# Kernel tuning notes

Hardware: AMD Instinct MI355X
Metric: run time of the kernel (lower is better)

Reference implementation:

```python
import math
import jax, jax.numpy as jnp
import numpy as np

N_ATOMS = 500000
N_TYPES = 16
N_FEAT = 64
N_CENTER = 40000
N_NEIGH = 6
H1, H2 = 128, 64
CUTOFF = 3.5
D_IN = 3 + 3 * N_FEAT  # 195

# static off-diagonal (j,k) pairs, row-major == torch's ~eye boolean mask order
_JJ, _KK = np.nonzero(~np.eye(N_NEIGH, dtype=bool))


def setup_inputs() -> dict:
    key = jax.random.key(0)
    ks = jax.random.split(key, 9)
    atoms_xyz = jax.random.normal(ks[0], (N_ATOMS, 3), dtype=jnp.float32) * 5.0
    atom_type_idx = jax.random.randint(ks[1], (N_ATOMS,), 0, N_TYPES)
    embed_table = jax.random.normal(ks[2], (N_TYPES, N_FEAT), dtype=jnp.float32)
    atom_i_idx = jax.random.randint(ks[3], (N_CENTER,), 0, N_ATOMS)
    # distinct neighbor indices per row (real neighbor lists never repeat an atom)
    base = jax.random.randint(ks[4], (N_CENTER, 1), 0, N_ATOMS)
    atom_j_idx = (base + jnp.arange(N_NEIGH)) % N_ATOMS
    # center->neighbor distances, strictly positive (within angular cutoff scale)
    dist_ij = 0.5 + 3.0 * jax.random.uniform(ks[5], (N_CENTER, N_NEIGH), dtype=jnp.float32)
    W1 = jax.random.normal(ks[6], (H1, D_IN), dtype=jnp.float32) / np.sqrt(D_IN).astype(np.float32)
    b1 = jnp.zeros((H1,), dtype=jnp.float32)
    W2 = jax.random.normal(ks[7], (H2, H1), dtype=jnp.float32) / np.sqrt(H1).astype(np.float32)
    b2 = jnp.zeros((H2,), dtype=jnp.float32)
    return dict(atoms_xyz=atoms_xyz, embed_table=embed_table, dist_ij=dist_ij,
                W1=W1, b1=b1, W2=W2, b2=b2,
                atom_type_idx=atom_type_idx, atom_i_idx=atom_i_idx, atom_j_idx=atom_j_idx)


def _ang_input(atoms_xyz, embed_table, dist_ij, atom_type_idx, atom_i_idx, atom_j_idx):
    # Build angular descriptor directly on off-diagonal (j,k) triples -> [C, T, 3+3F]
    xyz_j = atoms_xyz[atom_j_idx]                       # [C, N, 3]
    diff = xyz_j[:, _JJ] - xyz_j[:, _KK]                # [C, T, 3]
    d_jk = jnp.sqrt(jnp.sum(diff * diff, axis=-1))      # [C, T]
    dij = dist_ij[:, _JJ]                                # [C, T]
    dik = dist_ij[:, _KK]
    mx = jnp.maximum(dij, dik)
    mn = jnp.minimum(dij, dik)
    d_jk_norm = (d_jk - mx + mn) / (2.0 * mn)
    e_i = embed_table[atom_type_idx[atom_i_idx]]        # [C, F]
    e_n = embed_table[atom_type_idx[atom_j_idx]]        # [C, N, F]
    e_j = e_n[:, _JJ]                                    # [C, T, F]
    e_k = e_n[:, _KK]
    ang = jnp.concatenate([
        dij[..., None], dik[..., None], d_jk_norm[..., None],
        jnp.broadcast_to(e_i[:, None, :], e_j.shape),
        e_j / dij[..., None],
        e_k / dik[..., None],
    ], axis=-1)                                          # [C, T, 3+3F]
    return ang


def reference(atoms_xyz, embed_table, dist_ij, W1, b1, W2, b2,
              atom_type_idx, atom_i_idx, atom_j_idx):
    ang = _ang_input(atoms_xyz, embed_table, dist_ij,
                     atom_type_idx, atom_i_idx, atom_j_idx)   # [C, T, D_IN]
    C, T, _ = ang.shape
    x = ang.reshape(-1, D_IN)
    x = jax.nn.celu(x @ W1.T + b1)
    x = jax.nn.celu(x @ W2.T + b2)
    out = x.reshape(C, T, H2)
    # smooth angular cutoff from the ij, ik distance columns
    fc = 0.5 * jnp.cos(math.pi * jnp.clip(ang[:, :, 0:2] / CUTOFF, 0.0, 1.0)) + 0.5
    fc = jnp.prod(fc, axis=-1, keepdims=True)            # [C, T, 1]
    desc = jnp.sum(out * fc, axis=1)                     # [C, H2]
    return desc
```

## Files before the change

kernel.cpp:

```cpp
#include <hip/hip_runtime.h>
#include <hip/hip_bf16.h>

typedef __attribute__((ext_vector_type(8))) short bfrag;
typedef __attribute__((ext_vector_type(4))) float facc;
typedef __attribute__((ext_vector_type(4))) int ivec4;
typedef __attribute__((ext_vector_type(4))) short svec4;

#define DIN 195
#define H1 128
#define H2 64
#define CPB 4
#define ROWS 128
#define TPB 512
#define X1STR 136
#define TLSTR 40
#define VSTR 72

#define W1T_ELEMS (8*7*64*8)
#define W2T_ELEMS (4*4*64*8)

__device__ __forceinline__ short f2bf(float v) {
    __hip_bfloat16 h = __float2bfloat16(v);
    return __builtin_bit_cast(short, h);
}

__global__ void prep_weights(const float* __restrict__ W1, const float* __restrict__ W2,
                             __hip_bfloat16* __restrict__ W1t, __hip_bfloat16* __restrict__ W2t) {
    int i = blockIdx.x * 256 + threadIdx.x;
    if (i < W1T_ELEMS) {
        int e = i & 7, l = (i >> 3) & 63;
        int k0 = (i >> 9) % 7, mt = (i >> 9) / 7;
        int h = mt * 16 + (l & 15);
        int kp = k0 * 32 + ((l >> 4) & 3) * 8 + e;
        float v = 0.f;
        if (kp < 192)      v = W1[h * DIN + 3 + kp];
        else if (kp < 195) v = W1[h * DIN + (kp - 192)];
        W1t[i] = __float2bfloat16(v);
    } else {
        int j = i - W1T_ELEMS;
        if (j < W2T_ELEMS) {
            int e = j & 7, l = (j >> 3) & 63;
            int k0 = (j >> 9) & 3, mm = j >> 11;
            int h = mm * 16 + (l & 15);
            int k = k0 * 32 + ((l >> 4) & 3) * 8 + e;
            W2t[j] = __float2bfloat16(W2[h * H1 + k]);
        }
    }
}

template<bool PREP>
__global__ __launch_bounds__(TPB, 4) void angnet(
    const float* __restrict__ atoms_xyz,
    const float* __restrict__ embed,
    const float* __restrict__ dist_ij,
    const float* __restrict__ b1,
    const float* __restrict__ b2,
    const int* __restrict__ atype,
    const int* __restrict__ aidx,
    const int* __restrict__ ajdx,
    const __hip_bfloat16* __restrict__ W1t,
    const __hip_bfloat16* __restrict__ W2t,
    const float* __restrict__ W1f,
    const float* __restrict__ W2f,
    float* __restrict__ out)
{
    __shared__ __align__(16) __hip_bfloat16 x1s[ROWS][X1STR];
    __shared__ __align__(16) __hip_bfloat16 tail[ROWS][TLSTR];
    __shared__ __align__(16) __hip_bfloat16 vst[CPB][7][VSTR];
    __shared__ float fcs[ROWS];
    __shared__ float dstage[CPB][6];
    __shared__ float xyzs[CPB][6][3];
    __shared__ int   tidx[CPB][7];

    const int tid = threadIdx.x;
    const int C0 = blockIdx.x * CPB;

    {
        ivec4 zz = {0, 0, 0, 0};
        for (int i = tid; i < ROWS * TLSTR / 8; i += TPB)
            ((ivec4*)tail)[i] = zz;
    }
    if (tid < CPB * 7) {
        int c = tid / 7, r = tid % 7;
        tidx[c][r] = (r == 6) ? atype[aidx[C0 + c]] : atype[ajdx[(C0 + c) * 6 + r]];
    } else if (tid < CPB * 7 + CPB * 18) {
        int q = tid - CPB * 7; int c = q / 18, rr = q % 18; int n = rr / 3, ax = rr % 3;
        xyzs[c][n][ax] = atoms_xyz[(long)ajdx[(C0 + c) * 6 + n] * 3 + ax];
    } else if (tid < CPB * 7 + CPB * 18 + CPB * 6) {
        int q = tid - CPB * 7 - CPB * 18; int c = q / 6, n = q % 6;
        dstage[c][n] = dist_ij[(C0 + c) * 6 + n];
    }
    __syncthreads();

    if (tid < CPB * 7 * 8) {
        int c = tid / 56, rem = tid % 56, v = rem / 8, ch = rem % 8;
        int ti = tidx[c][v];
        float sc = (v < 6) ? (1.0f / dstage[c][v]) : 1.0f;
        const float* ep = &embed[ti * 64 + ch * 8];
        float4 e0 = *(const float4*)ep;
        float4 e1 = *(const float4*)(ep + 4);
        bfrag t;
        t[0] = f2bf(e0.x * sc); t[1] = f2bf(e0.y * sc);
        t[2] = f2bf(e0.z * sc); t[3] = f2bf(e0.w * sc);
        t[4] = f2bf(e1.x * sc); t[5] = f2bf(e1.y * sc);
        t[6] = f2bf(e1.z * sc); t[7] = f2bf(e1.w * sc);
        *(bfrag*)&vst[c][v][ch * 8] = t;
    } else if (tid >= 256 && tid < 256 + CPB * 30) {
        int q = tid - 256; int c = q / 30, t = q % 30;
        int j = t / 5, k2 = t - j * 5, k = k2 + (k2 >= j ? 1 : 0);
        float dij = dstage[c][j], dik = dstage[c][k];
        float dx = xyzs[c][j][0] - xyzs[c][k][0];
        float dy = xyzs[c][j][1] - xyzs[c][k][1];
        float dz = xyzs[c][j][2] - xyzs[c][k][2];
        float djk = sqrtf(dx * dx + dy * dy + dz * dz);
        float mx = fmaxf(dij, dik), mn = fminf(dij, dik);
        float djkn = (djk - mx + mn) / (2.0f * mn);
        int r = c * 32 + t;
        tail[r][0] = __float2bfloat16(dij);
        tail[r][1] = __float2bfloat16(dik);
        tail[r][2] = __float2bfloat16(djkn);
        const float PIF = 3.14159265358979323846f;
        float ca = __cosf(PIF * (dij * (1.0f / 3.5f)));
        float cb = __cosf(PIF * (dik * (1.0f / 3.5f)));
        fcs[r] = (0.5f * ca + 0.5f) * (0.5f * cb + 0.5f);
    } else if (tid >= 376 && tid < 384) {
        int p = tid - 376;
        fcs[(p >> 1) * 32 + 30 + (p & 1)] = 0.f;
    }
    __syncthreads();

    const int w = tid >> 6, l = tid & 63, lr = l & 15, lq = l >> 4;

    int jn[8], kn[8];
    #pragma unroll
    for (int n = 0; n < 8; ++n) {
        int t = (n & 1) * 16 + lr;
        int j = t / 5, k2 = t - j * 5, k = k2 + (k2 >= j ? 1 : 0);
        if (t >= 30) { j = 0; k = 0; }
        jn[n] = j; kn[n] = k;
    }
    facc a1[8];
    #pragma unroll
    for (int n = 0; n < 8; ++n) a1[n] = (facc){0.f, 0.f, 0.f, 0.f};

    #pragma unroll
    for (int k0 = 0; k0 < 7; ++k0) {
        bfrag Af;
        if (PREP) {
            Af = *(const bfrag*)&W1t[(w * 7 + k0) * 512 + l * 8];
        } else {
            #pragma unroll
            for (int e = 0; e < 8; ++e) {
                int kp = k0 * 32 + lq * 8 + e;
                int h = w * 16 + lr;
                float v = 0.f;
                if (kp < 192)      v = W1f[h * DIN + 3 + kp];
                else if (kp < 195) v = W1f[h * DIN + kp - 192];
                Af[e] = f2bf(v);
            }
        }
        #pragma unroll
        for (int n = 0; n < 8; ++n) {
            const __hip_bfloat16* bp;
            if (k0 < 2)      bp = &vst[n >> 1][6][(k0 & 1) * 32 + lq * 8];
            else if (k0 < 4) bp = &vst[n >> 1][jn[n]][(k0 & 1) * 32 + lq * 8];
            else if (k0 < 6) bp = &vst[n >> 1][kn[n]][(k0 & 1) * 32 + lq * 8];
            else             bp = &tail[n * 16 + lr][lq * 8];
            bfrag Bf = *(const bfrag*)bp;
            a1[n] = __builtin_amdgcn_mfma_f32_16x16x32_bf16(Af, Bf, a1[n], 0, 0, 0);
        }
    }

    {
        float b1v[4];
        #pragma unroll
        for (int g = 0; g < 4; ++g) b1v[g] = b1[w * 16 + lq * 4 + g];
        #pragma unroll
        for (int n = 0; n < 8; ++n) {
            svec4 pk;
            #pragma unroll
            for (int g = 0; g < 4; ++g) {
                float v = a1[n][g] + b1v[g];
                v = v > 0.f ? v : (__expf(v) - 1.f);
                pk[g] = f2bf(v);
            }
            *(svec4*)&x1s[n * 16 + lr][w * 16 + lq * 4] = pk;
        }
    }
    __syncthreads();

    const int mm = w & 3, q = w >> 2;
    facc a2[4];
    #pragma unroll
    for (int i = 0; i < 4; ++i) a2[i] = (facc){0.f, 0.f, 0.f, 0.f};

    #pragma unroll
    for (int k0 = 0; k0 < 4; ++k0) {
        bfrag Af;
        if (PREP) {
            Af = *(const bfrag*)&W2t[(mm * 4 + k0) * 512 + l * 8];
        } else {
            #pragma unroll
            for (int e = 0; e < 8; ++e)
                Af[e] = f2bf(W2f[(mm * 16 + lr) * H1 + k0 * 32 + lq * 8 + e]);
        }
        #pragma unroll
        for (int i = 0; i < 4; ++i) {
            bfrag Bf = *(const bfrag*)&x1s[(q * 4 + i) * 16 + lr][k0 * 32 + lq * 8];
            a2[i] = __builtin_amdgcn_mfma_f32_16x16x32_bf16(Af, Bf, a2[i], 0, 0, 0);
        }
    }

    {
        float b2v[4];
        #pragma unroll
        for (int g = 0; g < 4; ++g) b2v[g] = b2[mm * 16 + lq * 4 + g];
        float s[4][4];
        #pragma unroll
        for (int i = 0; i < 4; ++i) {
            float fr = fcs[(q * 4 + i) * 16 + lr];
            #pragma unroll
            for (int g = 0; g < 4; ++g) {
                float v = a2[i][g] + b2v[g];
                v = v > 0.f ? v : (__expf(v) - 1.f);
                s[i][g] = v * fr;
            }
        }
        #pragma unroll
        for (int st = 1; st < 16; st <<= 1) {
            #pragma unroll
            for (int i = 0; i < 4; ++i)
                #pragma unroll
                for (int g = 0; g < 4; ++g)
                    s[i][g] += __shfl_xor(s[i][g], st);
        }
        if (lr == 0) {
            #pragma unroll
            for (int u = 0; u < 2; ++u)
                #pragma unroll
                for (int g = 0; g < 4; ++g)
                    out[(long)(C0 + q * 2 + u) * 64 + mm * 16 + lq * 4 + g] = s[2 * u][g] + s[2 * u + 1][g];
        }
    }
}

extern "C" void kernel_launch(void* const* d_in, const int* in_sizes, int n_in,
                              void* d_out, int out_size, void* d_ws, size_t ws_size,
                              hipStream_t stream) {
    const float* atoms_xyz = (const float*)d_in[0];
    const float* embed     = (const float*)d_in[1];
    const float* dist_ij   = (const float*)d_in[2];
    const float* W1        = (const float*)d_in[3];
    const float* b1        = (const float*)d_in[4];
    const float* W2        = (const float*)d_in[5];
    const float* b2        = (const float*)d_in[6];
    const int*   atype     = (const int*)d_in[7];
    const int*   aidx      = (const int*)d_in[8];
    const int*   ajdx      = (const int*)d_in[9];
    float* out = (float*)d_out;

    const int n_center = in_sizes[8];
    const int n_blocks = n_center / CPB;

    size_t need = (size_t)(W1T_ELEMS + W2T_ELEMS) * sizeof(__hip_bfloat16);
    if (ws_size >= need) {
        __hip_bfloat16* W1t = (__hip_bfloat16*)d_ws;
        __hip_bfloat16* W2t = W1t + W1T_ELEMS;
        int prep_total = W1T_ELEMS + W2T_ELEMS;
        prep_weights<<<(prep_total + 255) / 256, 256, 0, stream>>>(W1, W2, W1t, W2t);
        angnet<true><<<n_blocks, TPB, 0, stream>>>(atoms_xyz, embed, dist_ij, b1, b2,
                                                   atype, aidx, ajdx, W1t, W2t, W1, W2, out);
    } else {
        angnet<false><<<n_blocks, TPB, 0, stream>>>(atoms_xyz, embed, dist_ij, b1, b2,
                                                    atype, aidx, ajdx, nullptr, nullptr, W1, W2, out);
    }
}
```

Before: 142.6 us.

## Shrink LDS footprint, fold bias into GEMM, transpose second GEMM for cheaper reduction

Removes the padded tail buffer by packing the three distance features plus a constant 1 into a 4-element row, and folds b1 into the W1 weight tile at column 195 so the bias add disappears. Staging data is aliased into x1s, and fcs is stored as bf16, which cuts shared memory per block. Launch bounds are raised to 8 blocks per SM to increase occupancy. The second GEMM is re-oriented so activations form the A operand, so the output reduction needs only two shuffles plus a small shared-memory pass. The costs are that the partial sums and cutoff weights are now rounded to bf16, which can lower accuracy, and the tighter launch bound may cause register spills.

```diff
diff --git a/kernel.cpp b/kernel.cpp
--- a/kernel.cpp
+++ b/kernel.cpp
@@ -4,6 +4,7 @@
 typedef __attribute__((ext_vector_type(8))) short bfrag;
 typedef __attribute__((ext_vector_type(4))) float facc;
 typedef __attribute__((ext_vector_type(4))) int ivec4;
+typedef __attribute__((ext_vector_type(2))) int ivec2;
 typedef __attribute__((ext_vector_type(4))) short svec4;
 
 #define DIN 195
@@ -13,7 +14,6 @@
 #define ROWS 128
 #define TPB 512
 #define X1STR 136
-#define TLSTR 40
 #define VSTR 72
 
 #define W1T_ELEMS (8*7*64*8)
@@ -23,8 +23,12 @@
     __hip_bfloat16 h = __float2bfloat16(v);
     return __builtin_bit_cast(short, h);
 }
+__device__ __forceinline__ float celu1(float v) {
+    return v > 0.f ? v : (__expf(v) - 1.f);
+}
 
 __global__ void prep_weights(const float* __restrict__ W1, const float* __restrict__ W2,
+                             const float* __restrict__ b1,
                              __hip_bfloat16* __restrict__ W1t, __hip_bfloat16* __restrict__ W2t) {
     int i = blockIdx.x * 256 + threadIdx.x;
     if (i < W1T_ELEMS) {
@@ -33,15 +37,16 @@
         int h = mt * 16 + (l & 15);
         int kp = k0 * 32 + ((l >> 4) & 3) * 8 + e;
         float v = 0.f;
-        if (kp < 192)      v = W1[h * DIN + 3 + kp];
-        else if (kp < 195) v = W1[h * DIN + (kp - 192)];
+        if (kp < 192)       v = W1[h * DIN + 3 + kp];
+        else if (kp < 195)  v = W1[h * DIN + (kp - 192)];
+        else if (kp == 195) v = b1[h];
         W1t[i] = __float2bfloat16(v);
     } else {
         int j = i - W1T_ELEMS;
         if (j < W2T_ELEMS) {
             int e = j & 7, l = (j >> 3) & 63;
-            int k0 = (j >> 9) & 3, mm = j >> 11;
-            int h = mm * 16 + (l & 15);
+            int k0 = (j >> 9) & 3, nt = j >> 11;
+            int h = nt * 16 + (l & 15);
             int k = k0 * 32 + ((l >> 4) & 3) * 8 + e;
             W2t[j] = __float2bfloat16(W2[h * H1 + k]);
         }
@@ -49,7 +54,7 @@
 }
 
 template<bool PREP>
-__global__ __launch_bounds__(TPB, 4) void angnet(
+__global__ __launch_bounds__(TPB, 8) void angnet(
     const float* __restrict__ atoms_xyz,
     const float* __restrict__ embed,
     const float* __restrict__ dist_ij,
@@ -65,37 +70,35 @@
     float* __restrict__ out)
 {
     __shared__ __align__(16) __hip_bfloat16 x1s[ROWS][X1STR];
-    __shared__ __align__(16) __hip_bfloat16 tail[ROWS][TLSTR];
     __shared__ __align__(16) __hip_bfloat16 vst[CPB][7][VSTR];
-    __shared__ float fcs[ROWS];
-    __shared__ float dstage[CPB][6];
-    __shared__ float xyzs[CPB][6][3];
-    __shared__ int   tidx[CPB][7];
+    __shared__ __align__(16) __hip_bfloat16 tvp[512];
+    __shared__ __hip_bfloat16 fcs[ROWS];
+
+    float* stg  = (float*)&x1s[0][0];
+    int*   tidxp = (int*)(stg + 96);
 
     const int tid = threadIdx.x;
     const int C0 = blockIdx.x * CPB;
 
-    {
+    if (tid < 64) {
         ivec4 zz = {0, 0, 0, 0};
-        for (int i = tid; i < ROWS * TLSTR / 8; i += TPB)
-            ((ivec4*)tail)[i] = zz;
-    }
-    if (tid < CPB * 7) {
-        int c = tid / 7, r = tid % 7;
-        tidx[c][r] = (r == 6) ? atype[aidx[C0 + c]] : atype[ajdx[(C0 + c) * 6 + r]];
-    } else if (tid < CPB * 7 + CPB * 18) {
-        int q = tid - CPB * 7; int c = q / 18, rr = q % 18; int n = rr / 3, ax = rr % 3;
-        xyzs[c][n][ax] = atoms_xyz[(long)ajdx[(C0 + c) * 6 + n] * 3 + ax];
-    } else if (tid < CPB * 7 + CPB * 18 + CPB * 6) {
-        int q = tid - CPB * 7 - CPB * 18; int c = q / 6, n = q % 6;
-        dstage[c][n] = dist_ij[(C0 + c) * 6 + n];
+        ((ivec4*)tvp)[tid] = zz;
+    } else if (tid >= 64 && tid < 92) {
+        int q = tid - 64, c = q / 7, r = q % 7;
+        tidxp[c * 7 + r] = (r == 6) ? atype[aidx[C0 + c]] : atype[ajdx[(C0 + c) * 6 + r]];
+    } else if (tid >= 96 && tid < 168) {
+        int q = tid - 96, c = q / 18, rr = q % 18, n = rr / 3, ax = rr % 3;
+        stg[c * 18 + n * 3 + ax] = atoms_xyz[(long)ajdx[(C0 + c) * 6 + n] * 3 + ax];
+    } else if (tid >= 168 && tid < 192) {
+        int q = tid - 168, c = q / 6, n = q % 6;
+        stg[72 + c * 6 + n] = dist_ij[(C0 + c) * 6 + n];
     }
     __syncthreads();
 
     if (tid < CPB * 7 * 8) {
         int c = tid / 56, rem = tid % 56, v = rem / 8, ch = rem % 8;
-        int ti = tidx[c][v];
-        float sc = (v < 6) ? (1.0f / dstage[c][v]) : 1.0f;
+        int ti = tidxp[c * 7 + v];
+        float sc = (v < 6) ? (1.0f / stg[72 + c * 6 + v]) : 1.0f;
         const float* ep = &embed[ti * 64 + ch * 8];
         float4 e0 = *(const float4*)ep;
         float4 e1 = *(const float4*)(ep + 4);
@@ -106,39 +109,39 @@
         t[6] = f2bf(e1.z * sc); t[7] = f2bf(e1.w * sc);
         *(bfrag*)&vst[c][v][ch * 8] = t;
     } else if (tid >= 256 && tid < 256 + CPB * 30) {
-        int q = tid - 256; int c = q / 30, t = q % 30;
+        int q = tid - 256, c = q / 30, t = q % 30;
         int j = t / 5, k2 = t - j * 5, k = k2 + (k2 >= j ? 1 : 0);
-        float dij = dstage[c][j], dik = dstage[c][k];
-        float dx = xyzs[c][j][0] - xyzs[c][k][0];
-        float dy = xyzs[c][j][1] - xyzs[c][k][1];
-        float dz = xyzs[c][j][2] - xyzs[c][k][2];
+        float dij = stg[72 + c * 6 + j], dik = stg[72 + c * 6 + k];
+        float dx = stg[c * 18 + j * 3 + 0] - stg[c * 18 + k * 3 + 0];
+        float dy = stg[c * 18 + j * 3 + 1] - stg[c * 18 + k * 3 + 1];
+        float dz = stg[c * 18 + j * 3 + 2] - stg[c * 18 + k * 3 + 2];
         float djk = sqrtf(dx * dx + dy * dy + dz * dz);
         float mx = fmaxf(dij, dik), mn = fminf(dij, dik);
         float djkn = (djk - mx + mn) / (2.0f * mn);
         int r = c * 32 + t;
-        tail[r][0] = __float2bfloat16(dij);
-        tail[r][1] = __float2bfloat16(dik);
-        tail[r][2] = __float2bfloat16(djkn);
+        svec4 pk;
+        pk[0] = f2bf(dij); pk[1] = f2bf(dik); pk[2] = f2bf(djkn); pk[3] = f2bf(1.0f);
+        *(svec4*)&tvp[r * 4] = pk;
         const float PIF = 3.14159265358979323846f;
         float ca = __cosf(PIF * (dij * (1.0f / 3.5f)));
         float cb = __cosf(PIF * (dik * (1.0f / 3.5f)));
-        fcs[r] = (0.5f * ca + 0.5f) * (0.5f * cb + 0.5f);
+        fcs[r] = __float2bfloat16((0.5f * ca + 0.5f) * (0.5f * cb + 0.5f));
     } else if (tid >= 376 && tid < 384) {
         int p = tid - 376;
-        fcs[(p >> 1) * 32 + 30 + (p & 1)] = 0.f;
+        fcs[(p >> 1) * 32 + 30 + (p & 1)] = __float2bfloat16(0.f);
     }
     __syncthreads();
 
     const int w = tid >> 6, l = tid & 63, lr = l & 15, lq = l >> 4;
 
-    int jn[8], kn[8];
-    #pragma unroll
-    for (int n = 0; n < 8; ++n) {
-        int t = (n & 1) * 16 + lr;
-        int j = t / 5, k2 = t - j * 5, k = k2 + (k2 >= j ? 1 : 0);
-        if (t >= 30) { j = 0; k = 0; }
-        jn[n] = j; kn[n] = k;
-    }
+    int jA = lr / 5, k2A = lr % 5; int kA = k2A + (k2A >= jA ? 1 : 0);
+    int tB = 16 + lr, jB = 0, kB = 0;
+    if (tB < 30) { jB = tB / 5; int k2B = tB % 5; kB = k2B + (k2B >= jB ? 1 : 0); }
+    const int joA = jA * VSTR, joB = jB * VSTR, koA = kA * VSTR, koB = kB * VSTR;
+    const __hip_bfloat16* vb[4];
+    #pragma unroll
+    for (int c = 0; c < 4; ++c) vb[c] = &vst[c][0][lq * 8];
+
     facc a1[8];
     #pragma unroll
     for (int n = 0; n < 8; ++n) a1[n] = (facc){0.f, 0.f, 0.f, 0.f};
@@ -154,93 +157,91 @@
                 int kp = k0 * 32 + lq * 8 + e;
                 int h = w * 16 + lr;
                 float v = 0.f;
-                if (kp < 192)      v = W1f[h * DIN + 3 + kp];
-                else if (kp < 195) v = W1f[h * DIN + kp - 192];
+                if (kp < 192)       v = W1f[h * DIN + 3 + kp];
+                else if (kp < 195)  v = W1f[h * DIN + kp - 192];
+                else if (kp == 195) v = b1[h];
                 Af[e] = f2bf(v);
             }
         }
         #pragma unroll
         for (int n = 0; n < 8; ++n) {
-            const __hip_bfloat16* bp;
-            if (k0 < 2)      bp = &vst[n >> 1][6][(k0 & 1) * 32 + lq * 8];
-            else if (k0 < 4) bp = &vst[n >> 1][jn[n]][(k0 & 1) * 32 + lq * 8];
-            else if (k0 < 6) bp = &vst[n >> 1][kn[n]][(k0 & 1) * 32 + lq * 8];
-            else             bp = &tail[n * 16 + lr][lq * 8];
-            bfrag Bf = *(const bfrag*)bp;
+            bfrag Bf;
+            if (k0 < 6) {
+                const __hip_bfloat16* bp;
+                if (k0 < 2)      bp = vb[n >> 1] + 6 * VSTR + (k0 & 1) * 32;
+                else if (k0 < 4) bp = vb[n >> 1] + ((n & 1) ? joB : joA) + (k0 & 1) * 32;
+                else             bp = vb[n >> 1] + ((n & 1) ? koB : koA) + (k0 & 1) * 32;
+                Bf = *(const bfrag*)bp;
+            } else {
+                svec4 tv = *(const svec4*)&tvp[(n * 16 + lr) * 4];
+                ivec2 ti = __builtin_bit_cast(ivec2, tv);
+                int lo = (lq == 0) ? ti[0] : 0;
+                int hi = (lq == 0) ? ti[1] : 0;
+                ivec4 bi = {lo, hi, 0, 0};
+                Bf = __builtin_bit_cast(bfrag, bi);
+            }
             a1[n] = __builtin_amdgcn_mfma_f32_16x16x32_bf16(Af, Bf, a1[n], 0, 0, 0);
         }
     }
 
+    #pragma unroll
+    for (int n = 0; n < 8; ++n) {
+        svec4 pk;
+        #pragma unroll
+        for (int g = 0; g < 4; ++g) pk[g] = f2bf(celu1(a1[n][g]));
+        *(svec4*)&x1s[n * 16 + lr][w * 16 + lq * 4] = pk;
+    }
+    __syncthreads();
+
+    facc a2[4];
+    #pragma unroll
+    for (int n = 0; n < 4; ++n) a2[n] = (facc){0.f, 0.f, 0.f, 0.f};
+
+    #pragma unroll
+    for (int k0 = 0; k0 < 4; ++k0) {
+        bfrag Af2 = *(const bfrag*)&x1s[w * 16 + lr][k0 * 32 + lq * 8];
+        #pragma unroll
+        for (int n = 0; n < 4; ++n) {
+            bfrag Bf2;
+            if (PREP) {
+                Bf2 = *(const bfrag*)&W2t[(n * 4 + k0) * 512 + l * 8];
+            } else {
+                #pragma unroll
+                for (int e = 0; e < 8; ++e)
+                    Bf2[e] = f2bf(W2f[(n * 16 + lr) * H1 + k0 * 32 + lq * 8 + e]);
+            }
+            a2[n] = __builtin_amdgcn_mfma_f32_16x16x32_bf16(Af2, Bf2, a2[n], 0, 0, 0);
+        }
+    }
+
     {
-        float b1v[4];
-        #pragma unroll
-        for (int g = 0; g < 4; ++g) b1v[g] = b1[w * 16 + lq * 4 + g];
-        #pragma unroll
-        for (int n = 0; n < 8; ++n) {
-            svec4 pk;
+        float fr[4];
+        #pragma unroll
+        for (int g = 0; g < 4; ++g) fr[g] = __bfloat162float(fcs[w * 16 + lq * 4 + g]);
+        float t[4];
+        #pragma unroll
+        for (int n = 0; n < 4; ++n) {
+            float b2v = b2[n * 16 + lr];
+            float s = 0.f;
             #pragma unroll
-            for (int g = 0; g < 4; ++g) {
-                float v = a1[n][g] + b1v[g];
-                v = v > 0.f ? v : (__expf(v) - 1.f);
-                pk[g] = f2bf(v);
-            }
-            *(svec4*)&x1s[n * 16 + lr][w * 16 + lq * 4] = pk;
-        }
-    }
-    __syncthreads();
-
-    const int mm = w & 3, q = w >> 2;
-    facc a2[4];
-    #pragma unroll
-    for (int i = 0; i < 4; ++i) a2[i] = (facc){0.f, 0.f, 0.f, 0.f};
-
-    #pragma unroll
-    for (int k0 = 0; k0 < 4; ++k0) {
-        bfrag Af;
-        if (PREP) {
-            Af = *(const bfrag*)&W2t[(mm * 4 + k0) * 512 + l * 8];
-        } else {
+            for (int g = 0; g < 4; ++g)
+                s += celu1(a2[n][g] + b2v) * fr[g];
+            s += __shfl_xor(s, 16);
+            s += __shfl_xor(s, 32);
+            t[n] = s;
+        }
+        if (lq == 0) {
             #pragma unroll
-            for (int e = 0; e < 8; ++e)
-                Af[e] = f2bf(W2f[(mm * 16 + lr) * H1 + k0 * 32 + lq * 8 + e]);
-        }
-        #pragma unroll
-        for (int i = 0; i < 4; ++i) {
-            bfrag Bf = *(const bfrag*)&x1s[(q * 4 + i) * 16 + lr][k0 * 32 + lq * 8];
-            a2[i] = __builtin_amdgcn_mfma_f32_16x16x32_bf16(Af, Bf, a2[i], 0, 0, 0);
-        }
-    }
-
-    {
-        float b2v[4];
-        #pragma unroll
-        for (int g = 0; g < 4; ++g) b2v[g] = b2[mm * 16 + lq * 4 + g];
-        float s[4][4];
-        #pragma unroll
-        for (int i = 0; i < 4; ++i) {
-            float fr = fcs[(q * 4 + i) * 16 + lr];
-            #pragma unroll
-            for (int g = 0; g < 4; ++g) {
-                float v = a2[i][g] + b2v[g];
-                v = v > 0.f ? v : (__expf(v) - 1.f);
-                s[i][g] = v * fr;
-            }
-        }
-        #pragma unroll
-        for (int st = 1; st < 16; st <<= 1) {
-            #pragma unroll
-            for (int i = 0; i < 4; ++i)
-                #pragma unroll
-                for (int g = 0; g < 4; ++g)
-                    s[i][g] += __shfl_xor(s[i][g], st);
-        }
-        if (lr == 0) {
-            #pragma unroll
-            for (int u = 0; u < 2; ++u)
-                #pragma unroll
-                for (int g = 0; g < 4; ++g)
-                    out[(long)(C0 + q * 2 + u) * 64 + mm * 16 + lq * 4 + g] = s[2 * u][g] + s[2 * u + 1][g];
-        }
+            for (int n = 0; n < 4; ++n)
+                tvp[w * 64 + n * 16 + lr] = __float2bfloat16(t[n]);
+        }
+    }
+    __syncthreads();
+
+    if (tid < 256) {
+        int c = tid >> 6, o = tid & 63;
+        out[(long)(C0 + c) * 64 + o] =
+            __bfloat162float(tvp[(2 * c) * 64 + o]) + __bfloat162float(tvp[(2 * c + 1) * 64 + o]);
     }
 }
 
@@ -267,7 +268,7 @@
         __hip_bfloat16* W1t = (__hip_bfloat16*)d_ws;
         __hip_bfloat16* W2t = W1t + W1T_ELEMS;
         int prep_total = W1T_ELEMS + W2T_ELEMS;
-        prep_weights<<<(prep_total + 255) / 256, 256, 0, stream>>>(W1, W2, W1t, W2t);
+        prep_weights<<<(prep_total + 255) / 256, 256, 0, stream>>>(W1, W2, b1, W1t, W2t);
         angnet<true><<<n_blocks, TPB, 0, stream>>>(atoms_xyz, embed, dist_ij, b1, b2,
                                                    atype, aidx, ajdx, W1t, W2t, W1, W2, out);
     } else {
```

New measurement: 119.2 us. 1.2x faster.
